# Kernel tuning notes

Measured on AMD Instinct MI355X. Metric: run time of the kernel, lower is better.

Reference implementation:

```python
import jax, jax.numpy as jnp
import numpy as np

B, P, D, N, K = 8, 784, 1536, 20000, 9


def setup_inputs() -> dict:
    key = jax.random.key(0)
    k1, k2 = jax.random.split(key)
    x = jax.random.normal(k1, (B, P, D), dtype=jnp.float32)       # patch embeddings [B, P, D]
    memory = jax.random.normal(k2, (N, D), dtype=jnp.float32)     # FAISS memory bank [N, D]
    return {"x": x, "memory": memory, "k": K}


def reference(x, memory, k):
    # Squared L2 distances (FAISS IndexFlatL2 convention): [B, P, N]
    x2 = jnp.sum(x * x, axis=-1, keepdims=True)                   # [B, P, 1]
    m2 = jnp.sum(memory * memory, axis=-1)                        # [N]
    d = x2 + m2[None, None, :] - 2.0 * jnp.einsum('bpd,nd->bpn', x, memory)
    # k nearest (smallest distances, ascending) -> score_patches [B, P, k]
    neg_topk, _ = jax.lax.top_k(-d, k)
    score_patches = -neg_topk
    closest_dist = score_patches[..., 0]                          # [B, P]
    idxmax = jnp.argmax(closest_dist, axis=1)                     # [B]
    # N_b: the k neighbor distances of the worst (max closest-dist) patch
    N_b = jnp.take_along_axis(score_patches, idxmax[:, None, None], axis=1)[:, 0, :]  # [B, k]
    N_b = N_b - jnp.max(N_b, axis=1, keepdims=True)               # numerical stabilization (as in source)
    N_b_exp = jnp.exp(N_b)
    w = 1.0 - jnp.max(N_b_exp, axis=1) / jnp.sum(N_b_exp, axis=1)  # [B]
    score = w * jnp.max(closest_dist, axis=1)                      # [B]
    return score
```

## Files before the change

kernel.cpp:

```cpp
#include <hip/hip_runtime.h>
#include <hip/hip_fp8.h>
#include <math.h>

#define B_    8
#define P_    784
#define M_    6272
#define D_    1536
#define N_    20000
#define NC_   8

#define MPAD  6400
#define NPAD2 20224
#define MT2   25
#define NT2   79
#define KT2   12

#define NBLK  625

using i32x8  = __attribute__((ext_vector_type(8))) int;
using f32x4v = __attribute__((ext_vector_type(4))) float;

#define GLD_LDS16(src, dst)                                            \
  __builtin_amdgcn_global_load_lds(                                    \
      (__attribute__((address_space(1))) const void*)(src),            \
      (__attribute__((address_space(3))) void*)(dst), 16, 0, 0)

__device__ __forceinline__ unsigned char f2fp8(float v) {
  __hip_fp8_e4m3 q(v);
  return (unsigned char)q.__x;
}

__device__ __forceinline__ unsigned fenc(float f) {
  unsigned u = __float_as_uint(f);
  return (u >> 31) ? ~u : (u | 0x80000000u);
}
__device__ __forceinline__ float fdec(unsigned k) {
  return (k >> 31) ? __uint_as_float(k & 0x7FFFFFFFu) : __uint_as_float(~k);
}

__device__ __forceinline__ void convert_one(const float* __restrict__ src,
                                            unsigned char* __restrict__ dst,
                                            float* __restrict__ sq,
                                            int row, int realrows) {
  const int t = threadIdx.x;
  if (row >= realrows) {
    unsigned* w = (unsigned*)(dst + (size_t)row * D_);
    for (int i = t; i < D_ / 4; i += 256) w[i] = 0u;
    if (t == 0) sq[row] = 1e30f;
    return;
  }
  const float4* r4 = (const float4*)(src + (size_t)row * D_);
  unsigned* w = (unsigned*)(dst + (size_t)row * D_);
  float s = 0.f;
  for (int i = t; i < D_ / 4; i += 256) {
    float4 v = r4[i];
    s += v.x * v.x + v.y * v.y + v.z * v.z + v.w * v.w;
    unsigned pk = (unsigned)f2fp8(v.x) | ((unsigned)f2fp8(v.y) << 8) |
                  ((unsigned)f2fp8(v.z) << 16) | ((unsigned)f2fp8(v.w) << 24);
    w[i] = pk;
  }
#pragma unroll
  for (int m = 32; m >= 1; m >>= 1) s += __shfl_xor(s, m);
  __shared__ float ws4[4];
  if ((t & 63) == 0) ws4[t >> 6] = s;
  __syncthreads();
  if (t == 0) sq[row] = ws4[0] + ws4[1] + ws4[2] + ws4[3];
}

__global__ void convert_all(const float* __restrict__ x, const float* __restrict__ mem,
                            unsigned char* __restrict__ xq, unsigned char* __restrict__ mq,
                            float* __restrict__ x2, float* __restrict__ m2) {
  const int blk = blockIdx.x;
  if (blk < NPAD2) convert_one(mem, mq, m2, blk, N_);
  else convert_one(x, xq, x2, blk - NPAD2, M_);
}

__global__ __launch_bounds__(512, 2) void gemm_min8(
    const unsigned char* __restrict__ xq, const unsigned char* __restrict__ mq,
    const float* __restrict__ m2, unsigned* __restrict__ closest_enc) {
  __shared__ __attribute__((aligned(16))) char ldsFlat[131072];
  __shared__ float ldsMin[4][256];

  const int NWG = MT2 * NT2;
  const int bid = blockIdx.x;
  const int q = NWG >> 3, r = NWG & 7;
  const int xcd = bid & 7, loc = bid >> 3;
  const int wg = (xcd < r ? xcd * (q + 1) : r * (q + 1) + (xcd - r) * q) + loc;
  const int s = wg / (5 * NT2);
  const int r2 = wg - s * (5 * NT2);
  const int mT = s * 5 + (r2 % 5);
  const int nT = r2 / 5;

  const int tid = threadIdx.x;
  const int lane = tid & 63, wid = tid >> 6;
  const int wm = wid >> 2, wn = wid & 3;
  const int g = lane >> 4, r16 = lane & 15;
  const int mBase = mT * 256, nBase = nT * 256;

  const int stRow = wid * 8 + (lane >> 3);
  const int stA = mBase + stRow;
  const int stB = nBase + stRow;
  const int cswz16 = ((lane & 7) ^ ((lane >> 3) & 7)) * 16;

  const int csl = (g * 32) ^ ((r16 & 7) << 4);
  const int csh = csl ^ 16;
  const int rdA = wm * 16384 + r16 * 128;
  const int rdB = wn * 8192 + r16 * 128;

#define STAGE(matsel, srcp, rowb, bufb, h, ktv) do {                        \
    char* dst_ = ldsFlat + (matsel) * 65536 + (bufb) * 32768 +              \
                 (h) * 16384 + wid * 1024;                                  \
    const unsigned char* s_ =                                               \
        (srcp) + (size_t)((rowb) + (h) * 128) * 1536 + (ktv) * 128 + cswz16;\
    GLD_LDS16(s_, dst_);                                                    \
    GLD_LDS16(s_ + 64 * 1536, dst_ + 8192);                                 \
  } while (0)

#define LDFRAG(base, off) ({                                                \
    int4 lo_ = *(const int4*)((base) + (off) + csl);                        \
    int4 hi_ = *(const int4*)((base) + (off) + csh);                        \
    i32x8{lo_.x, lo_.y, lo_.z, lo_.w, hi_.x, hi_.y, hi_.z, hi_.w}; })

#define MFMA8(a, b, c) __builtin_amdgcn_mfma_scale_f32_16x16x128_f8f6f4(    \
    (a), (b), (c), 0, 0, 0, 0x7F7F7F7F, 0, 0x7F7F7F7F)

  f32x4v acc[8][4];
#pragma unroll
  for (int i = 0; i < 8; ++i)
#pragma unroll
    for (int j = 0; j < 4; ++j) acc[i][j] = f32x4v{0.f, 0.f, 0.f, 0.f};

  STAGE(1, mq, stB, 0, 0, 0);
  STAGE(1, mq, stB, 0, 1, 0);
  STAGE(0, xq, stA, 0, 0, 0);
  STAGE(0, xq, stA, 0, 1, 0);
  STAGE(1, mq, stB, 1, 0, 1);
  STAGE(1, mq, stB, 1, 1, 1);
  asm volatile("s_waitcnt vmcnt(4)");
  __builtin_amdgcn_s_barrier();
  __builtin_amdgcn_sched_barrier(0);

#pragma unroll 1
  for (int kt = 0; kt < KT2; ++kt) {
    const int bufc = kt & 1;
    const char* Ab = ldsFlat + bufc * 32768;
    const char* Bb = ldsFlat + 65536 + bufc * 32768;
    const bool stgA = (kt + 1) < KT2;
    const bool stgB = (kt + 2) < KT2;
    i32x8 bf[4], af[4];

#pragma unroll
    for (int nf = 0; nf < 4; ++nf) bf[nf] = LDFRAG(Bb, rdB + nf * 2048);
#pragma unroll
    for (int mf = 0; mf < 4; ++mf) af[mf] = LDFRAG(Ab, rdA + mf * 2048);
    if (stgA) {
      STAGE(0, xq, stA, bufc ^ 1, 0, kt + 1);
      STAGE(0, xq, stA, bufc ^ 1, 1, kt + 1);
    }
    __builtin_amdgcn_s_barrier();
    asm volatile("s_waitcnt lgkmcnt(0)");
    __builtin_amdgcn_s_setprio(1);
#pragma unroll
    for (int mf = 0; mf < 4; ++mf)
#pragma unroll
      for (int nf = 0; nf < 4; ++nf)
        acc[mf][nf] = MFMA8(af[mf], bf[nf], acc[mf][nf]);
    __builtin_amdgcn_s_setprio(0);
    __builtin_amdgcn_s_barrier();

#pragma unroll
    for (int mf = 0; mf < 4; ++mf) af[mf] = LDFRAG(Ab, rdA + (mf + 4) * 2048);
    if (stgB) {
      STAGE(1, mq, stB, bufc, 0, kt + 2);
      STAGE(1, mq, stB, bufc, 1, kt + 2);
    }
    __builtin_amdgcn_s_barrier();
    asm volatile("s_waitcnt lgkmcnt(0)");
    __builtin_amdgcn_s_setprio(1);
#pragma unroll
    for (int mf = 0; mf < 4; ++mf)
#pragma unroll
      for (int nf = 0; nf < 4; ++nf)
        acc[mf + 4][nf] = MFMA8(af[mf], bf[nf], acc[mf + 4][nf]);
    __builtin_amdgcn_s_setprio(0);
    if (kt >= KT2 - 2) {
      asm volatile("s_waitcnt vmcnt(0)");
    } else {
      asm volatile("s_waitcnt vmcnt(4)");
    }
    __builtin_amdgcn_s_barrier();
    __builtin_amdgcn_sched_barrier(0);
  }
#undef STAGE
#undef LDFRAG
#undef MFMA8

  float m2v[4];
#pragma unroll
  for (int nf = 0; nf < 4; ++nf) m2v[nf] = m2[nBase + wn * 64 + nf * 16 + r16];
#pragma unroll
  for (int mf = 0; mf < 8; ++mf) {
    float mn[4];
#pragma unroll
    for (int i = 0; i < 4; ++i) {
      float v = m2v[0] - 2.f * acc[mf][0][i];
      v = fminf(v, m2v[1] - 2.f * acc[mf][1][i]);
      v = fminf(v, m2v[2] - 2.f * acc[mf][2][i]);
      v = fminf(v, m2v[3] - 2.f * acc[mf][3][i]);
      mn[i] = v;
    }
#pragma unroll
    for (int msk = 1; msk < 16; msk <<= 1)
#pragma unroll
      for (int i = 0; i < 4; ++i) mn[i] = fminf(mn[i], __shfl_xor(mn[i], msk));
    if (r16 == 0)
#pragma unroll
      for (int i = 0; i < 4; ++i)
        ldsMin[wn][wm * 128 + mf * 16 + g * 4 + i] = mn[i];
  }
  __syncthreads();
  if (tid < 256) {
    float v = fminf(fminf(ldsMin[0][tid], ldsMin[1][tid]),
                    fminf(ldsMin[2][tid], ldsMin[3][tid]));
    atomicMin(&closest_enc[mBase + tid], fenc(v));
  }
}

__global__ void topcand_kernel(const unsigned* __restrict__ closest_enc,
                               const float* __restrict__ x2,
                               int* __restrict__ cand) {
  const int b = blockIdx.x;
  const int t = threadIdx.x;
  __shared__ float cls[P_];
  for (int p = t; p < P_; p += 256) {
    const int row = b * P_ + p;
    cls[p] = x2[row] + fdec(closest_enc[row]);
  }
  __syncthreads();
  __shared__ float wv[4];
  __shared__ int wi_[4];
  __shared__ int picked[NC_];
  for (int r = 0; r < NC_; ++r) {
    float mv = -3e38f; int mi = 1 << 30;
    for (int p = t; p < P_; p += 256) {
      bool skip = false;
      for (int c = 0; c < r; ++c) skip |= (picked[c] == p);
      float v = cls[p];
      if (!skip && (v > mv || (v == mv && p < mi))) { mv = v; mi = p; }
    }
#pragma unroll
    for (int m = 32; m >= 1; m >>= 1) {
      float ov = __shfl_xor(mv, m); int oi = __shfl_xor(mi, m);
      if (ov > mv || (ov == mv && oi < mi)) { mv = ov; mi = oi; }
    }
    if ((t & 63) == 0) { wv[t >> 6] = mv; wi_[t >> 6] = mi; }
    __syncthreads();
    if (t == 0) {
      float bv = wv[0]; int bi = wi_[0];
      for (int w = 1; w < 4; ++w)
        if (wv[w] > bv || (wv[w] == bv && wi_[w] < bi)) { bv = wv[w]; bi = wi_[w]; }
      picked[r] = bi;
      cand[b * NC_ + r] = bi;
    }
    __syncthreads();
  }
}

__device__ __forceinline__ void ins9(float* t, float v) {
  if (v < t[8]) {
    int p = 8;
    while (p > 0 && t[p - 1] > v) { t[p] = t[p - 1]; --p; }
    t[p] = v;
  }
}

__global__ __launch_bounds__(256) void cand_dist9(
    const float* __restrict__ x, const float* __restrict__ mem,
    const float* __restrict__ x2, const float* __restrict__ m2,
    const int* __restrict__ cand, float* __restrict__ ctop) {
  const int wid = threadIdx.x >> 6, lane = threadIdx.x & 63;
  const int blk = blockIdx.x;
  __shared__ float ldsD[B_ * NC_][36];

  for (int batch = 0; batch < 2; ++batch) {
    const int rbase = blk * 32 + wid * 8 + batch * 4;
    float4 m4[4][6];
    float m2r[4];
#pragma unroll
    for (int k = 0; k < 4; ++k) {
      const float4* mrow = (const float4*)(mem + (size_t)(rbase + k) * D_);
#pragma unroll
      for (int j = 0; j < 6; ++j) m4[k][j] = mrow[j * 64 + lane];
      m2r[k] = m2[rbase + k];
    }
    for (int bc = 0; bc < B_ * NC_; ++bc) {
      const int b = bc / NC_;
      const int p = cand[bc];
      const float4* xp = (const float4*)(x + ((size_t)b * P_ + p) * D_);
      float s0 = 0.f, s1 = 0.f, s2 = 0.f, s3 = 0.f;
#pragma unroll
      for (int j = 0; j < 6; ++j) {
        float4 a = xp[j * 64 + lane];
        s0 += a.x * m4[0][j].x + a.y * m4[0][j].y + a.z * m4[0][j].z + a.w * m4[0][j].w;
        s1 += a.x * m4[1][j].x + a.y * m4[1][j].y + a.z * m4[1][j].z + a.w * m4[1][j].w;
        s2 += a.x * m4[2][j].x + a.y * m4[2][j].y + a.z * m4[2][j].z + a.w * m4[2][j].w;
        s3 += a.x * m4[3][j].x + a.y * m4[3][j].y + a.z * m4[3][j].z + a.w * m4[3][j].w;
      }
#pragma unroll
      for (int msk = 32; msk >= 1; msk >>= 1) {
        s0 += __shfl_xor(s0, msk); s1 += __shfl_xor(s1, msk);
        s2 += __shfl_xor(s2, msk); s3 += __shfl_xor(s3, msk);
      }
      if (lane == 0) {
        const float xx = x2[b * P_ + p];
        const int rloc = wid * 8 + batch * 4;
        ldsD[bc][rloc + 0] = xx + m2r[0] - 2.f * s0;
        ldsD[bc][rloc + 1] = xx + m2r[1] - 2.f * s1;
        ldsD[bc][rloc + 2] = xx + m2r[2] - 2.f * s2;
        ldsD[bc][rloc + 3] = xx + m2r[3] - 2.f * s3;
      }
    }
  }
  __syncthreads();
  if (lane < 16) {
    const int bc = wid * 16 + lane;
    float t[9];
#pragma unroll
    for (int i = 0; i < 9; ++i) t[i] = 3e38f;
    for (int i = 0; i < 32; ++i) ins9(t, ldsD[bc][i]);
    float* o = ctop + ((size_t)bc * NBLK + blk) * 9;
#pragma unroll
    for (int i = 0; i < 9; ++i) o[i] = t[i];
  }
}

__global__ void merge_top9(const float* __restrict__ ctop, float* __restrict__ top9) {
  const int bc = blockIdx.x;
  const float* d = ctop + (size_t)bc * (NBLK * 9);
  float t[9];
#pragma unroll
  for (int i = 0; i < 9; ++i) t[i] = 3e38f;
  for (int n = threadIdx.x; n < NBLK * 9; n += 256) ins9(t, d[n]);
  __shared__ float l9[256 * 9];
  __shared__ float l9b[32 * 9];
  for (int i = 0; i < 9; ++i) l9[threadIdx.x * 9 + i] = t[i];
  __syncthreads();
  if (threadIdx.x < 32) {
    float u[9];
#pragma unroll
    for (int i = 0; i < 9; ++i) u[i] = 3e38f;
    for (int s = 0; s < 8; ++s)
      for (int i = 0; i < 9; ++i) ins9(u, l9[(threadIdx.x * 8 + s) * 9 + i]);
    for (int i = 0; i < 9; ++i) l9b[threadIdx.x * 9 + i] = u[i];
  }
  __syncthreads();
  if (threadIdx.x == 0) {
    float u[9];
#pragma unroll
    for (int i = 0; i < 9; ++i) u[i] = 3e38f;
    for (int s = 0; s < 32; ++s)
      for (int i = 0; i < 9; ++i) ins9(u, l9b[s * 9 + i]);
    for (int i = 0; i < 9; ++i) top9[bc * 9 + i] = u[i];
  }
}

__global__ void score_kernel(const float* __restrict__ top9, const int* __restrict__ cand,
                             float* __restrict__ out) {
  const int b = threadIdx.x;
  if (b >= B_) return;
  float bestv = -3e38f; int bestc = 0, bestp = 1 << 30;
  for (int c = 0; c < NC_; ++c) {
    float v = top9[(b * NC_ + c) * 9 + 0];
    int p = cand[b * NC_ + c];
    if (v > bestv || (v == bestv && p < bestp)) { bestv = v; bestc = c; bestp = p; }
  }
  const float* v9 = &top9[(b * NC_ + bestc) * 9];
  float mx = v9[8];
  float sum = 0.f, mxe = 0.f;
  for (int i = 0; i < 9; ++i) {
    float e = expf(v9[i] - mx);
    sum += e;
    if (e > mxe) mxe = e;
  }
  out[b] = (1.f - mxe / sum) * bestv;
}

extern "C" void kernel_launch(void* const* d_in, const int* in_sizes, int n_in,
                              void* d_out, int out_size, void* d_ws, size_t ws_size,
                              hipStream_t stream) {
  const float* x = (const float*)d_in[0];
  const float* mem = (const float*)d_in[1];
  float* out = (float*)d_out;
  char* ws = (char*)d_ws;

  unsigned char* xq    = (unsigned char*)(ws);
  unsigned char* mq    = (unsigned char*)(ws + 9830400);
  float* x2            = (float*)(ws + 40894464);
  float* m2            = (float*)(ws + 40920064);
  unsigned* closest_enc= (unsigned*)(ws + 41000960);
  int*   cand          = (int*)  (ws + 41026560);
  float* ctop          = (float*)(ws + 41026816);
  float* top9          = (float*)(ws + 42466816);

  hipMemsetAsync(closest_enc, 0xFF, MPAD * 4, stream);
  convert_all<<<NPAD2 + MPAD, 256, 0, stream>>>(x, mem, xq, mq, x2, m2);
  gemm_min8<<<MT2 * NT2, 512, 0, stream>>>(xq, mq, m2, closest_enc);
  topcand_kernel<<<B_, 256, 0, stream>>>(closest_enc, x2, cand);
  cand_dist9<<<NBLK, 256, 0, stream>>>(x, mem, x2, m2, cand, ctop);
  merge_top9<<<B_ * NC_, 256, 0, stream>>>(ctop, top9);
  score_kernel<<<1, 64, 0, stream>>>(top9, cand, out);
}
```

Baseline: 494.5 us.

## Shrink GEMM tiles to 128x128 with higher occupancy and hardware fp8 pack conversion

```diff
diff --git a/kernel.cpp b/kernel.cpp
--- a/kernel.cpp
+++ b/kernel.cpp
@@ -1,5 +1,4 @@
 #include <hip/hip_runtime.h>
-#include <hip/hip_fp8.h>
 #include <math.h>
 
 #define B_    8
@@ -11,9 +10,9 @@
 
 #define MPAD  6400
 #define NPAD2 20224
-#define MT2   25
-#define NT2   79
-#define KT2   12
+#define MTg   50
+#define NTg   158
+#define KTg   12
 
 #define NBLK  625
 
@@ -24,11 +23,6 @@
   __builtin_amdgcn_global_load_lds(                                    \
       (__attribute__((address_space(1))) const void*)(src),            \
       (__attribute__((address_space(3))) void*)(dst), 16, 0, 0)
-
-__device__ __forceinline__ unsigned char f2fp8(float v) {
-  __hip_fp8_e4m3 q(v);
-  return (unsigned char)q.__x;
-}
 
 __device__ __forceinline__ unsigned fenc(float f) {
   unsigned u = __float_as_uint(f);
@@ -55,9 +49,9 @@
   for (int i = t; i < D_ / 4; i += 256) {
     float4 v = r4[i];
     s += v.x * v.x + v.y * v.y + v.z * v.z + v.w * v.w;
-    unsigned pk = (unsigned)f2fp8(v.x) | ((unsigned)f2fp8(v.y) << 8) |
-                  ((unsigned)f2fp8(v.z) << 16) | ((unsigned)f2fp8(v.w) << 24);
-    w[i] = pk;
+    int pk = __builtin_amdgcn_cvt_pk_fp8_f32(v.x, v.y, 0, false);
+    pk     = __builtin_amdgcn_cvt_pk_fp8_f32(v.z, v.w, pk, true);
+    w[i] = (unsigned)pk;
   }
 #pragma unroll
   for (int m = 32; m >= 1; m >>= 1) s += __shfl_xor(s, m);
@@ -75,45 +69,50 @@
   else convert_one(x, xq, x2, blk - NPAD2, M_);
 }
 
-__global__ __launch_bounds__(512, 2) void gemm_min8(
+__global__ __launch_bounds__(512, 4) void gemm_min8(
     const unsigned char* __restrict__ xq, const unsigned char* __restrict__ mq,
     const float* __restrict__ m2, unsigned* __restrict__ closest_enc) {
-  __shared__ __attribute__((aligned(16))) char ldsFlat[131072];
-  __shared__ float ldsMin[4][256];
-
-  const int NWG = MT2 * NT2;
+  __shared__ __attribute__((aligned(16))) char ldsFlat[65536];
+  __shared__ float ldsMin[4][128];
+
+  const int NWG = MTg * NTg;
   const int bid = blockIdx.x;
   const int q = NWG >> 3, r = NWG & 7;
   const int xcd = bid & 7, loc = bid >> 3;
   const int wg = (xcd < r ? xcd * (q + 1) : r * (q + 1) + (xcd - r) * q) + loc;
-  const int s = wg / (5 * NT2);
-  const int r2 = wg - s * (5 * NT2);
-  const int mT = s * 5 + (r2 % 5);
-  const int nT = r2 / 5;
+  const int FT = 6 * 8 * NTg;
+  int mT, nT;
+  if (wg < FT) {
+    int s = wg / (8 * NTg);
+    int r2 = wg - s * (8 * NTg);
+    mT = s * 8 + (r2 & 7);
+    nT = r2 >> 3;
+  } else {
+    int rem = wg - FT;
+    mT = 48 + (rem & 1);
+    nT = rem >> 1;
+  }
 
   const int tid = threadIdx.x;
   const int lane = tid & 63, wid = tid >> 6;
   const int wm = wid >> 2, wn = wid & 3;
   const int g = lane >> 4, r16 = lane & 15;
-  const int mBase = mT * 256, nBase = nT * 256;
-
-  const int stRow = wid * 8 + (lane >> 3);
-  const int stA = mBase + stRow;
-  const int stB = nBase + stRow;
+  const int mBase = mT * 128, nBase = nT * 128;
+
   const int cswz16 = ((lane & 7) ^ ((lane >> 3) & 7)) * 16;
 
   const int csl = (g * 32) ^ ((r16 & 7) << 4);
   const int csh = csl ^ 16;
-  const int rdA = wm * 16384 + r16 * 128;
-  const int rdB = wn * 8192 + r16 * 128;
-
-#define STAGE(matsel, srcp, rowb, bufb, h, ktv) do {                        \
-    char* dst_ = ldsFlat + (matsel) * 65536 + (bufb) * 32768 +              \
-                 (h) * 16384 + wid * 1024;                                  \
+  const int rdA = wm * 8192 + r16 * 128;
+  const int rdB = wn * 4096 + r16 * 128;
+
+#define STAGE(msel, srcp, tbase, bufb, ktv) do {                            \
+    char* dst_ = ldsFlat + (msel) * 32768 + (bufb) * 16384 + wid * 2048;    \
     const unsigned char* s_ =                                               \
-        (srcp) + (size_t)((rowb) + (h) * 128) * 1536 + (ktv) * 128 + cswz16;\
+        (srcp) + (size_t)((tbase) + wid * 16 + (lane >> 3)) * 1536 +        \
+        (ktv) * 128 + cswz16;                                               \
     GLD_LDS16(s_, dst_);                                                    \
-    GLD_LDS16(s_ + 64 * 1536, dst_ + 8192);                                 \
+    GLD_LDS16(s_ + 8 * 1536, dst_ + 1024);                                  \
   } while (0)
 
 #define LDFRAG(base, off) ({                                                \
@@ -124,70 +123,45 @@
 #define MFMA8(a, b, c) __builtin_amdgcn_mfma_scale_f32_16x16x128_f8f6f4(    \
     (a), (b), (c), 0, 0, 0, 0x7F7F7F7F, 0, 0x7F7F7F7F)
 
-  f32x4v acc[8][4];
-#pragma unroll
-  for (int i = 0; i < 8; ++i)
-#pragma unroll
-    for (int j = 0; j < 4; ++j) acc[i][j] = f32x4v{0.f, 0.f, 0.f, 0.f};
-
-  STAGE(1, mq, stB, 0, 0, 0);
-  STAGE(1, mq, stB, 0, 1, 0);
-  STAGE(0, xq, stA, 0, 0, 0);
-  STAGE(0, xq, stA, 0, 1, 0);
-  STAGE(1, mq, stB, 1, 0, 1);
-  STAGE(1, mq, stB, 1, 1, 1);
-  asm volatile("s_waitcnt vmcnt(4)");
+  f32x4v acc[4][2];
+#pragma unroll
+  for (int i = 0; i < 4; ++i)
+#pragma unroll
+    for (int j = 0; j < 2; ++j) acc[i][j] = f32x4v{0.f, 0.f, 0.f, 0.f};
+
+  STAGE(0, xq, mBase, 0, 0);
+  STAGE(1, mq, nBase, 0, 0);
+  asm volatile("s_waitcnt vmcnt(0)");
   __builtin_amdgcn_s_barrier();
   __builtin_amdgcn_sched_barrier(0);
 
 #pragma unroll 1
-  for (int kt = 0; kt < KT2; ++kt) {
+  for (int kt = 0; kt < KTg; ++kt) {
     const int bufc = kt & 1;
-    const char* Ab = ldsFlat + bufc * 32768;
-    const char* Bb = ldsFlat + 65536 + bufc * 32768;
-    const bool stgA = (kt + 1) < KT2;
-    const bool stgB = (kt + 2) < KT2;
-    i32x8 bf[4], af[4];
-
-#pragma unroll
-    for (int nf = 0; nf < 4; ++nf) bf[nf] = LDFRAG(Bb, rdB + nf * 2048);
+    const char* Ab = ldsFlat + bufc * 16384;
+    const char* Bb = ldsFlat + 32768 + bufc * 16384;
+
+    if (kt + 1 < KTg) {
+      STAGE(0, xq, mBase, bufc ^ 1, kt + 1);
+      STAGE(1, mq, nBase, bufc ^ 1, kt + 1);
+    }
+
+    i32x8 bf[2], af[4];
+#pragma unroll
+    for (int nf = 0; nf < 2; ++nf) bf[nf] = LDFRAG(Bb, rdB + nf * 2048);
 #pragma unroll
     for (int mf = 0; mf < 4; ++mf) af[mf] = LDFRAG(Ab, rdA + mf * 2048);
-    if (stgA) {
-      STAGE(0, xq, stA, bufc ^ 1, 0, kt + 1);
-      STAGE(0, xq, stA, bufc ^ 1, 1, kt + 1);
-    }
+
     __builtin_amdgcn_s_barrier();
     asm volatile("s_waitcnt lgkmcnt(0)");
     __builtin_amdgcn_s_setprio(1);
 #pragma unroll
     for (int mf = 0; mf < 4; ++mf)
 #pragma unroll
-      for (int nf = 0; nf < 4; ++nf)
+      for (int nf = 0; nf < 2; ++nf)
         acc[mf][nf] = MFMA8(af[mf], bf[nf], acc[mf][nf]);
     __builtin_amdgcn_s_setprio(0);
-    __builtin_amdgcn_s_barrier();
-
-#pragma unroll
-    for (int mf = 0; mf < 4; ++mf) af[mf] = LDFRAG(Ab, rdA + (mf + 4) * 2048);
-    if (stgB) {
-      STAGE(1, mq, stB, bufc, 0, kt + 2);
-      STAGE(1, mq, stB, bufc, 1, kt + 2);
-    }
-    __builtin_amdgcn_s_barrier();
-    asm volatile("s_waitcnt lgkmcnt(0)");
-    __builtin_amdgcn_s_setprio(1);
-#pragma unroll
-    for (int mf = 0; mf < 4; ++mf)
-#pragma unroll
-      for (int nf = 0; nf < 4; ++nf)
-        acc[mf + 4][nf] = MFMA8(af[mf], bf[nf], acc[mf + 4][nf]);
-    __builtin_amdgcn_s_setprio(0);
-    if (kt >= KT2 - 2) {
-      asm volatile("s_waitcnt vmcnt(0)");
-    } else {
-      asm volatile("s_waitcnt vmcnt(4)");
-    }
+    asm volatile("s_waitcnt vmcnt(0)");
     __builtin_amdgcn_s_barrier();
     __builtin_amdgcn_sched_barrier(0);
   }
@@ -195,20 +169,15 @@
 #undef LDFRAG
 #undef MFMA8
 
-  float m2v[4];
-#pragma unroll
-  for (int nf = 0; nf < 4; ++nf) m2v[nf] = m2[nBase + wn * 64 + nf * 16 + r16];
-#pragma unroll
-  for (int mf = 0; mf < 8; ++mf) {
+  float m2v[2];
+#pragma unroll
+  for (int nf = 0; nf < 2; ++nf) m2v[nf] = m2[nBase + wn * 32 + nf * 16 + r16];
+#pragma unroll
+  for (int mf = 0; mf < 4; ++mf) {
     float mn[4];
 #pragma unroll
-    for (int i = 0; i < 4; ++i) {
-      float v = m2v[0] - 2.f * acc[mf][0][i];
-      v = fminf(v, m2v[1] - 2.f * acc[mf][1][i]);
-      v = fminf(v, m2v[2] - 2.f * acc[mf][2][i]);
-      v = fminf(v, m2v[3] - 2.f * acc[mf][3][i]);
-      mn[i] = v;
-    }
+    for (int i = 0; i < 4; ++i)
+      mn[i] = fminf(m2v[0] - 2.f * acc[mf][0][i], m2v[1] - 2.f * acc[mf][1][i]);
 #pragma unroll
     for (int msk = 1; msk < 16; msk <<= 1)
 #pragma unroll
@@ -216,10 +185,10 @@
     if (r16 == 0)
 #pragma unroll
       for (int i = 0; i < 4; ++i)
-        ldsMin[wn][wm * 128 + mf * 16 + g * 4 + i] = mn[i];
-  }
-  __syncthreads();
-  if (tid < 256) {
+        ldsMin[wn][wm * 64 + mf * 16 + g * 4 + i] = mn[i];
+  }
+  __syncthreads();
+  if (tid < 128) {
     float v = fminf(fminf(ldsMin[0][tid], ldsMin[1][tid]),
                     fminf(ldsMin[2][tid], ldsMin[3][tid]));
     atomicMin(&closest_enc[mBase + tid], fenc(v));
@@ -404,7 +373,7 @@
 
   hipMemsetAsync(closest_enc, 0xFF, MPAD * 4, stream);
   convert_all<<<NPAD2 + MPAD, 256, 0, stream>>>(x, mem, xq, mq, x2, m2);
-  gemm_min8<<<MT2 * NT2, 512, 0, stream>>>(xq, mq, m2, closest_enc);
+  gemm_min8<<<MTg * NTg, 512, 0, stream>>>(xq, mq, m2, closest_enc);
   topcand_kernel<<<B_, 256, 0, stream>>>(closest_enc, x2, cand);
   cand_dist9<<<NBLK, 256, 0, stream>>>(x, mem, x2, m2, cand, ctop);
   merge_top9<<<B_ * NC_, 256, 0, stream>>>(ctop, top9);
```

Measured after the change: 559.3 us. 1.13x slower.
